# Kernel tuning notes

Hardware: AMD Instinct MI355X
Metric: run time of the kernel (lower is better)

The kernel has to match this reference:

```python
import jax, jax.numpy as jnp
import numpy as np

K = 512        # num_embeddings
D = 64         # embedding_dim
BETA = 0.25
B, S = 64, 4096


def setup_inputs() -> dict:
    key = jax.random.key(0)
    k1, k2 = jax.random.split(key)
    latents = jax.random.normal(k1, (B, S, D), dtype=jnp.float32)
    # torch init: uniform_(-1/K, 1/K)
    embedding = jax.random.uniform(k2, (K, D), dtype=jnp.float32,
                                   minval=-1.0 / K, maxval=1.0 / K)
    return {"latents": latents, "embedding": embedding}


def reference(latents, embedding):
    d = embedding.shape[1]
    flat = latents.reshape(-1, d)                       # [N, D]
    # squared-euclidean distances via norm expansion: [N, K]
    dist = (jnp.sum(flat * flat, axis=1, keepdims=True)
            + jnp.sum(embedding * embedding, axis=1)
            - 2.0 * flat @ embedding.T)
    inds = jnp.argmin(dist, axis=1)                     # [N] (channel = identity)
    # one-hot @ codebook == gather; same math, no [N,K] one-hot materialized
    quantized = embedding[inds].reshape(latents.shape)  # [B, S, D]
    commitment_loss = jnp.mean((jax.lax.stop_gradient(quantized) - latents) ** 2)
    embedding_loss = jnp.mean((quantized - jax.lax.stop_gradient(latents)) ** 2)
    vq_loss = commitment_loss * BETA + embedding_loss
    # straight-through estimator
    quantized_st = latents + jax.lax.stop_gradient(quantized - latents)
    return quantized_st, vq_loss
```

## Files before the change

kernel.cpp:

```cpp
#include <hip/hip_runtime.h>
#include <math.h>
#include <stdint.h>

#define KCODES 512
#define DIM 64
#define NROWS (64 * 4096)
#define BLOCK 512
#define GROUP_ROWS 32
#define ROWS_PER_WAVE 64
#define BM ((BLOCK / 64) * ROWS_PER_WAVE)
#define NBLK (NROWS / BM)

typedef __bf16 bf16x8 __attribute__((ext_vector_type(8)));
typedef float f32x4 __attribute__((ext_vector_type(4)));

typedef __attribute__((address_space(3))) uint32_t* lds_ptr_t;
typedef const __attribute__((address_space(1))) uint32_t* glb_ptr_t;

__global__ void vq_prep_kernel(const float* __restrict__ emb,
                               float* __restrict__ en1,
                               __bf16* __restrict__ ebf) {
    int k = blockIdx.x * blockDim.x + threadIdx.x;
    if (k >= KCODES) return;
    const float4* e4 = reinterpret_cast<const float4*>(emb + k * DIM);
    float s0 = 0.f, s1 = 0.f, s2 = 0.f, s3 = 0.f;
#pragma unroll
    for (int j = 0; j < 8; ++j) {
        float4 v0 = e4[j * 2];
        float4 v1 = e4[j * 2 + 1];
        s0 = fmaf(v0.x, v0.x, s0); s1 = fmaf(v0.y, v0.y, s1);
        s2 = fmaf(v0.z, v0.z, s2); s3 = fmaf(v0.w, v0.w, s3);
        s0 = fmaf(v1.x, v1.x, s0); s1 = fmaf(v1.y, v1.y, s1);
        s2 = fmaf(v1.z, v1.z, s2); s3 = fmaf(v1.w, v1.w, s3);
        bf16x8 p;
        p[0] = (__bf16)(-2.f * v0.x); p[1] = (__bf16)(-2.f * v0.y);
        p[2] = (__bf16)(-2.f * v0.z); p[3] = (__bf16)(-2.f * v0.w);
        p[4] = (__bf16)(-2.f * v1.x); p[5] = (__bf16)(-2.f * v1.y);
        p[6] = (__bf16)(-2.f * v1.z); p[7] = (__bf16)(-2.f * v1.w);
        *reinterpret_cast<bf16x8*>(&ebf[k * DIM + (j ^ (k & 7)) * 8]) = p;
    }
    en1[k] = 1.0f + (s0 + s1) + (s2 + s3);
}

__launch_bounds__(BLOCK, 4)
__global__ void vq_mfma_kernel(const float* __restrict__ lat,
                               const float* __restrict__ emb,
                               const float* __restrict__ en1,
                               const __bf16* __restrict__ ebf,
                               float* __restrict__ outq,
                               float* __restrict__ partials) {
    __shared__ __align__(16) __bf16 e_lds[KCODES * DIM];
    __shared__ float en_lds[KCODES];
    __shared__ float wsum_lds[BLOCK / 64];

    const int t = threadIdx.x;
    const int lane = t & 63, wid = t >> 6;
    const int l15 = lane & 15, lq = lane >> 4;
    const int swz = l15 & 7;
    const uint32_t waverow = (uint32_t)blockIdx.x * BM + (uint32_t)wid * ROWS_PER_WAVE;

#pragma unroll
    for (int i = 0; i < 8; ++i) {
        int c = t + i * BLOCK;
        __builtin_amdgcn_global_load_lds(
            (glb_ptr_t)(const void*)(ebf + c * 8),
            (lds_ptr_t)(void*)(&e_lds[c * 8]), 16, 0, 0);
    }

    float4 araw[2][2][2];
    auto load_a = [&](int g) {
#pragma unroll
        for (int mf = 0; mf < 2; ++mf)
#pragma unroll
            for (int ks = 0; ks < 2; ++ks) {
                const float* xp = lat +
                    (waverow + (uint32_t)g * GROUP_ROWS + mf * 16 + l15) * DIM +
                    ks * 32 + lq * 8;
                araw[mf][ks][0] = reinterpret_cast<const float4*>(xp)[0];
                araw[mf][ks][1] = reinterpret_cast<const float4*>(xp)[1];
            }
    };

    load_a(0);
    en_lds[t] = en1[t];
    __syncthreads();

    float xsq = 0.f, lsum = 0.f;
    bf16x8 afrag[2][2];
    uint32_t best[2][4];

    auto cvt_a = [&]() {
#pragma unroll
        for (int mf = 0; mf < 2; ++mf)
#pragma unroll
            for (int ks = 0; ks < 2; ++ks) {
                float4 v0 = araw[mf][ks][0], v1 = araw[mf][ks][1];
                xsq = fmaf(v0.x, v0.x, xsq); xsq = fmaf(v0.y, v0.y, xsq);
                xsq = fmaf(v0.z, v0.z, xsq); xsq = fmaf(v0.w, v0.w, xsq);
                xsq = fmaf(v1.x, v1.x, xsq); xsq = fmaf(v1.y, v1.y, xsq);
                xsq = fmaf(v1.z, v1.z, xsq); xsq = fmaf(v1.w, v1.w, xsq);
                bf16x8 a;
                a[0] = (__bf16)v0.x; a[1] = (__bf16)v0.y;
                a[2] = (__bf16)v0.z; a[3] = (__bf16)v0.w;
                a[4] = (__bf16)v1.x; a[5] = (__bf16)v1.y;
                a[6] = (__bf16)v1.z; a[7] = (__bf16)v1.w;
                afrag[mf][ks] = a;
            }
    };

    auto score = [&]() {
#pragma unroll
        for (int mf = 0; mf < 2; ++mf)
#pragma unroll
            for (int r = 0; r < 4; ++r) best[mf][r] = 0xFFFFFFFFu;
#pragma unroll 4
        for (int nf = 0; nf < 32; ++nf) {
            const int n = nf * 16 + l15;
            bf16x8 b0 = *reinterpret_cast<const bf16x8*>(
                &e_lds[n * DIM + (lq ^ swz) * 8]);
            bf16x8 b1 = *reinterpret_cast<const bf16x8*>(
                &e_lds[n * DIM + ((lq + 4) ^ swz) * 8]);
            float en = en_lds[n];
            f32x4 acc0 = {en, en, en, en};
            f32x4 acc1 = {en, en, en, en};
            acc0 = __builtin_amdgcn_mfma_f32_16x16x32_bf16(afrag[0][0], b0, acc0, 0, 0, 0);
            acc0 = __builtin_amdgcn_mfma_f32_16x16x32_bf16(afrag[0][1], b1, acc0, 0, 0, 0);
            acc1 = __builtin_amdgcn_mfma_f32_16x16x32_bf16(afrag[1][0], b0, acc1, 0, 0, 0);
            acc1 = __builtin_amdgcn_mfma_f32_16x16x32_bf16(afrag[1][1], b1, acc1, 0, 0, 0);
            const uint32_t nn = (uint32_t)n;
#pragma unroll
            for (int r = 0; r < 4; ++r) {
                uint32_t k0 = (__float_as_uint(acc0[r]) & 0xFFFFFE00u) | nn;
                uint32_t k1 = (__float_as_uint(acc1[r]) & 0xFFFFFE00u) | nn;
                best[0][r] = min(best[0][r], k0);
                best[1][r] = min(best[1][r], k1);
            }
        }
    };

    auto finish = [&](int g) {
#pragma unroll
        for (int off = 1; off < 16; off <<= 1) {
#pragma unroll
            for (int mf = 0; mf < 2; ++mf)
#pragma unroll
                for (int r = 0; r < 4; ++r) {
                    uint32_t o = (uint32_t)__shfl_xor((int)best[mf][r], off, 64);
                    best[mf][r] = min(best[mf][r], o);
                }
        }
        if (l15 == 0) {
#pragma unroll
            for (int mf = 0; mf < 2; ++mf)
#pragma unroll
                for (int r = 0; r < 4; ++r)
                    lsum += __uint_as_float(best[mf][r] & 0xFFFFFE00u) - 1.0f;
        }
        const float4* emb4 = reinterpret_cast<const float4*>(emb);
        float4* out4 = reinterpret_cast<float4*>(outq);
#pragma unroll
        for (int mf = 0; mf < 2; ++mf) {
#pragma unroll
            for (int r = 0; r < 4; ++r) {
                const uint32_t k = best[mf][r] & 511u;
                const uint32_t grow =
                    waverow + (uint32_t)g * GROUP_ROWS + mf * 16 + lq * 4 + r;
                float4 e4 = emb4[k * 16 + l15];
                out4[grow * 16 + l15] = e4;
            }
        }
    };

    cvt_a();
    load_a(1);
    score();
    finish(0);
    cvt_a();
    score();
    finish(1);

    lsum += xsq;

#pragma unroll
    for (int off = 32; off > 0; off >>= 1)
        lsum += __shfl_down(lsum, off, 64);
    if (lane == 0) wsum_lds[wid] = lsum;
    __syncthreads();
    if (t == 0) {
        float s = 0.f;
#pragma unroll
        for (int w = 0; w < BLOCK / 64; ++w) s += wsum_lds[w];
        partials[blockIdx.x] = s;
    }
}

__global__ void vq_loss_kernel(const float* __restrict__ partials,
                               float* __restrict__ loss) {
    float s = 0.f;
    for (int i = threadIdx.x; i < NBLK; i += 256) s += partials[i];
#pragma unroll
    for (int off = 32; off > 0; off >>= 1)
        s += __shfl_down(s, off, 64);
    __shared__ float wsum[4];
    const int lane = threadIdx.x & 63;
    const int wid = threadIdx.x >> 6;
    if (lane == 0) wsum[wid] = s;
    __syncthreads();
    if (threadIdx.x == 0) {
        float tsum = 0.f;
#pragma unroll
        for (int w = 0; w < 4; ++w) tsum += wsum[w];
        loss[0] = 1.25f * (tsum / (float)((size_t)NROWS * DIM));
    }
}

extern "C" void kernel_launch(void* const* d_in, const int* in_sizes, int n_in,
                              void* d_out, int out_size, void* d_ws, size_t ws_size,
                              hipStream_t stream) {
    const float* lat = (const float*)d_in[0];
    const float* emb = (const float*)d_in[1];
    float* outq = (float*)d_out;
    float* loss = (float*)d_out + (size_t)NROWS * DIM;

    float* en1 = (float*)d_ws;
    __bf16* ebf = (__bf16*)((char*)d_ws + 2048);
    float* partials = (float*)((char*)d_ws + 67584);

    vq_prep_kernel<<<2, 256, 0, stream>>>(emb, en1, ebf);
    vq_mfma_kernel<<<NBLK, BLOCK, 0, stream>>>(lat, emb, en1, ebf, outq, partials);
    vq_loss_kernel<<<1, 256, 0, stream>>>(partials, loss);
}
```

Before: 40.90 us.

## Split codebook gather into separate kernel via stored best-code indices

The score kernel no longer writes quantized rows. It stores a 16-bit best-code index per row in workspace, and a new grid-stride gather kernel reads those indices and writes the embedding rows with coalesced float4 stores. The aim is to take the scattered output writes out of the compute-heavy MFMA kernel so it can overlap better, and to let the gather run at full memory bandwidth. The cost is an extra kernel launch plus a small index round-trip through memory.

```diff
diff --git a/kernel.cpp b/kernel.cpp
--- a/kernel.cpp
+++ b/kernel.cpp
@@ -10,6 +10,10 @@
 #define ROWS_PER_WAVE 64
 #define BM ((BLOCK / 64) * ROWS_PER_WAVE)
 #define NBLK (NROWS / BM)
+
+#define GBLOCK 256
+#define GGRID 2048
+#define GCHUNKS 8
 
 typedef __bf16 bf16x8 __attribute__((ext_vector_type(8)));
 typedef float f32x4 __attribute__((ext_vector_type(4)));
@@ -43,12 +47,11 @@
 }
 
 __launch_bounds__(BLOCK, 4)
-__global__ void vq_mfma_kernel(const float* __restrict__ lat,
-                               const float* __restrict__ emb,
-                               const float* __restrict__ en1,
-                               const __bf16* __restrict__ ebf,
-                               float* __restrict__ outq,
-                               float* __restrict__ partials) {
+__global__ void vq_score_kernel(const float* __restrict__ lat,
+                                const float* __restrict__ en1,
+                                const __bf16* __restrict__ ebf,
+                                ushort* __restrict__ bestk,
+                                float* __restrict__ partials) {
     __shared__ __align__(16) __bf16 e_lds[KCODES * DIM];
     __shared__ float en_lds[KCODES];
     __shared__ float wsum_lds[BLOCK / 64];
@@ -150,23 +153,18 @@
                 }
         }
         if (l15 == 0) {
-#pragma unroll
-            for (int mf = 0; mf < 2; ++mf)
+            const uint32_t rbase = waverow + (uint32_t)g * GROUP_ROWS + lq * 4;
+#pragma unroll
+            for (int mf = 0; mf < 2; ++mf) {
 #pragma unroll
                 for (int r = 0; r < 4; ++r)
                     lsum += __uint_as_float(best[mf][r] & 0xFFFFFE00u) - 1.0f;
-        }
-        const float4* emb4 = reinterpret_cast<const float4*>(emb);
-        float4* out4 = reinterpret_cast<float4*>(outq);
-#pragma unroll
-        for (int mf = 0; mf < 2; ++mf) {
-#pragma unroll
-            for (int r = 0; r < 4; ++r) {
-                const uint32_t k = best[mf][r] & 511u;
-                const uint32_t grow =
-                    waverow + (uint32_t)g * GROUP_ROWS + mf * 16 + lq * 4 + r;
-                float4 e4 = emb4[k * 16 + l15];
-                out4[grow * 16 + l15] = e4;
+                ushort4 s;
+                s.x = (ushort)(best[mf][0] & 511u);
+                s.y = (ushort)(best[mf][1] & 511u);
+                s.z = (ushort)(best[mf][2] & 511u);
+                s.w = (ushort)(best[mf][3] & 511u);
+                *reinterpret_cast<ushort4*>(&bestk[rbase + mf * 16]) = s;
             }
         }
     };
@@ -191,6 +189,34 @@
 #pragma unroll
         for (int w = 0; w < BLOCK / 64; ++w) s += wsum_lds[w];
         partials[blockIdx.x] = s;
+    }
+}
+
+__launch_bounds__(GBLOCK, 8)
+__global__ void vq_gather_kernel(const ushort* __restrict__ bestk,
+                                 const float* __restrict__ emb,
+                                 float* __restrict__ outq) {
+    const uint32_t tid = blockIdx.x * GBLOCK + threadIdx.x;
+    const uint32_t stride = GGRID * GBLOCK;
+    const float4* emb4 = reinterpret_cast<const float4*>(emb);
+    float4* out4 = reinterpret_cast<float4*>(outq);
+
+    uint32_t kk[GCHUNKS];
+#pragma unroll
+    for (int i = 0; i < GCHUNKS; ++i) {
+        uint32_t c = tid + i * stride;
+        kk[i] = bestk[c >> 4];
+    }
+    float4 v[GCHUNKS];
+#pragma unroll
+    for (int i = 0; i < GCHUNKS; ++i) {
+        uint32_t c = tid + i * stride;
+        v[i] = emb4[kk[i] * 16u + (c & 15u)];
+    }
+#pragma unroll
+    for (int i = 0; i < GCHUNKS; ++i) {
+        uint32_t c = tid + i * stride;
+        out4[c] = v[i];
     }
 }
 
@@ -225,8 +251,10 @@
     float* en1 = (float*)d_ws;
     __bf16* ebf = (__bf16*)((char*)d_ws + 2048);
     float* partials = (float*)((char*)d_ws + 67584);
+    ushort* bestk = (ushort*)((char*)d_ws + 69632);
 
     vq_prep_kernel<<<2, 256, 0, stream>>>(emb, en1, ebf);
-    vq_mfma_kernel<<<NBLK, BLOCK, 0, stream>>>(lat, emb, en1, ebf, outq, partials);
+    vq_score_kernel<<<NBLK, BLOCK, 0, stream>>>(lat, en1, ebf, bestk, partials);
+    vq_gather_kernel<<<GGRID, GBLOCK, 0, stream>>>(bestk, emb, outq);
     vq_loss_kernel<<<1, 256, 0, stream>>>(partials, loss);
 }
```

Measured after the change: 49.54 us. 21.1% more time.

## Score 64 rows per wave in one pass with 256-thread blocks and block remap

Applied to the files above, without the earlier changes.

Each wave now loads all 64 rows up front and scores them against the codebook in a single pass with four M-fragments, so each LDS B-fragment read feeds twice as many MFMAs. The block shrinks to 256 threads (so the codebook LDS fill loop doubles per thread), occupancy bounds drop to 2, and block IDs are permuted in an interleaved pattern. This removes the two-group software pipeline and doubles per-block codebook LDS loads relative to rows, at the cost of more registers and less latency hiding of the latent loads.

```diff
diff --git a/kernel.cpp b/kernel.cpp
--- a/kernel.cpp
+++ b/kernel.cpp
@@ -5,8 +5,7 @@
 #define KCODES 512
 #define DIM 64
 #define NROWS (64 * 4096)
-#define BLOCK 512
-#define GROUP_ROWS 32
+#define BLOCK 256
 #define ROWS_PER_WAVE 64
 #define BM ((BLOCK / 64) * ROWS_PER_WAVE)
 #define NBLK (NROWS / BM)
@@ -42,7 +41,7 @@
     en1[k] = 1.0f + (s0 + s1) + (s2 + s3);
 }
 
-__launch_bounds__(BLOCK, 4)
+__launch_bounds__(BLOCK, 2)
 __global__ void vq_mfma_kernel(const float* __restrict__ lat,
                                const float* __restrict__ emb,
                                const float* __restrict__ en1,
@@ -57,127 +56,112 @@
     const int lane = t & 63, wid = t >> 6;
     const int l15 = lane & 15, lq = lane >> 4;
     const int swz = l15 & 7;
-    const uint32_t waverow = (uint32_t)blockIdx.x * BM + (uint32_t)wid * ROWS_PER_WAVE;
-
-#pragma unroll
-    for (int i = 0; i < 8; ++i) {
+
+    const uint32_t bid = (blockIdx.x & 7) * (NBLK / 8) + (blockIdx.x >> 3);
+    const uint32_t waverow = bid * BM + (uint32_t)wid * ROWS_PER_WAVE;
+
+#pragma unroll
+    for (int i = 0; i < 16; ++i) {
         int c = t + i * BLOCK;
         __builtin_amdgcn_global_load_lds(
             (glb_ptr_t)(const void*)(ebf + c * 8),
             (lds_ptr_t)(void*)(&e_lds[c * 8]), 16, 0, 0);
     }
 
-    float4 araw[2][2][2];
-    auto load_a = [&](int g) {
-#pragma unroll
-        for (int mf = 0; mf < 2; ++mf)
-#pragma unroll
-            for (int ks = 0; ks < 2; ++ks) {
-                const float* xp = lat +
-                    (waverow + (uint32_t)g * GROUP_ROWS + mf * 16 + l15) * DIM +
-                    ks * 32 + lq * 8;
-                araw[mf][ks][0] = reinterpret_cast<const float4*>(xp)[0];
-                araw[mf][ks][1] = reinterpret_cast<const float4*>(xp)[1];
+    float4 araw[4][2][2];
+#pragma unroll
+    for (int mf = 0; mf < 4; ++mf) {
+#pragma unroll
+        for (int ks = 0; ks < 2; ++ks) {
+            const float* xp = lat +
+                (waverow + mf * 16 + l15) * DIM + ks * 32 + lq * 8;
+            araw[mf][ks][0] = reinterpret_cast<const float4*>(xp)[0];
+            araw[mf][ks][1] = reinterpret_cast<const float4*>(xp)[1];
+        }
+    }
+    en_lds[t] = en1[t];
+    en_lds[t + BLOCK] = en1[t + BLOCK];
+    __syncthreads();
+
+    float xsq = 0.f, lsum = 0.f;
+    bf16x8 afrag[4][2];
+#pragma unroll
+    for (int mf = 0; mf < 4; ++mf) {
+#pragma unroll
+        for (int ks = 0; ks < 2; ++ks) {
+            float4 v0 = araw[mf][ks][0], v1 = araw[mf][ks][1];
+            xsq = fmaf(v0.x, v0.x, xsq); xsq = fmaf(v0.y, v0.y, xsq);
+            xsq = fmaf(v0.z, v0.z, xsq); xsq = fmaf(v0.w, v0.w, xsq);
+            xsq = fmaf(v1.x, v1.x, xsq); xsq = fmaf(v1.y, v1.y, xsq);
+            xsq = fmaf(v1.z, v1.z, xsq); xsq = fmaf(v1.w, v1.w, xsq);
+            bf16x8 a;
+            a[0] = (__bf16)v0.x; a[1] = (__bf16)v0.y;
+            a[2] = (__bf16)v0.z; a[3] = (__bf16)v0.w;
+            a[4] = (__bf16)v1.x; a[5] = (__bf16)v1.y;
+            a[6] = (__bf16)v1.z; a[7] = (__bf16)v1.w;
+            afrag[mf][ks] = a;
+        }
+    }
+
+    uint32_t best[4][4];
+#pragma unroll
+    for (int mf = 0; mf < 4; ++mf)
+#pragma unroll
+        for (int r = 0; r < 4; ++r) best[mf][r] = 0xFFFFFFFFu;
+
+#pragma unroll 4
+    for (int nf = 0; nf < 32; ++nf) {
+        const int n = nf * 16 + l15;
+        bf16x8 b0 = *reinterpret_cast<const bf16x8*>(
+            &e_lds[n * DIM + (lq ^ swz) * 8]);
+        bf16x8 b1 = *reinterpret_cast<const bf16x8*>(
+            &e_lds[n * DIM + ((lq + 4) ^ swz) * 8]);
+        float en = en_lds[n];
+        const uint32_t nn = (uint32_t)n;
+#pragma unroll
+        for (int mf = 0; mf < 4; ++mf) {
+            f32x4 acc = {en, en, en, en};
+            acc = __builtin_amdgcn_mfma_f32_16x16x32_bf16(afrag[mf][0], b0, acc, 0, 0, 0);
+            acc = __builtin_amdgcn_mfma_f32_16x16x32_bf16(afrag[mf][1], b1, acc, 0, 0, 0);
+#pragma unroll
+            for (int r = 0; r < 4; ++r) {
+                uint32_t k = (__float_as_uint(acc[r]) & 0xFFFFFE00u) | nn;
+                best[mf][r] = min(best[mf][r], k);
             }
-    };
-
-    load_a(0);
-    en_lds[t] = en1[t];
-    __syncthreads();
-
-    float xsq = 0.f, lsum = 0.f;
-    bf16x8 afrag[2][2];
-    uint32_t best[2][4];
-
-    auto cvt_a = [&]() {
-#pragma unroll
-        for (int mf = 0; mf < 2; ++mf)
-#pragma unroll
-            for (int ks = 0; ks < 2; ++ks) {
-                float4 v0 = araw[mf][ks][0], v1 = araw[mf][ks][1];
-                xsq = fmaf(v0.x, v0.x, xsq); xsq = fmaf(v0.y, v0.y, xsq);
-                xsq = fmaf(v0.z, v0.z, xsq); xsq = fmaf(v0.w, v0.w, xsq);
-                xsq = fmaf(v1.x, v1.x, xsq); xsq = fmaf(v1.y, v1.y, xsq);
-                xsq = fmaf(v1.z, v1.z, xsq); xsq = fmaf(v1.w, v1.w, xsq);
-                bf16x8 a;
-                a[0] = (__bf16)v0.x; a[1] = (__bf16)v0.y;
-                a[2] = (__bf16)v0.z; a[3] = (__bf16)v0.w;
-                a[4] = (__bf16)v1.x; a[5] = (__bf16)v1.y;
-                a[6] = (__bf16)v1.z; a[7] = (__bf16)v1.w;
-                afrag[mf][ks] = a;
+        }
+    }
+
+#pragma unroll
+    for (int off = 1; off < 16; off <<= 1) {
+#pragma unroll
+        for (int mf = 0; mf < 4; ++mf)
+#pragma unroll
+            for (int r = 0; r < 4; ++r) {
+                uint32_t o = (uint32_t)__shfl_xor((int)best[mf][r], off, 64);
+                best[mf][r] = min(best[mf][r], o);
             }
-    };
-
-    auto score = [&]() {
-#pragma unroll
-        for (int mf = 0; mf < 2; ++mf)
-#pragma unroll
-            for (int r = 0; r < 4; ++r) best[mf][r] = 0xFFFFFFFFu;
-#pragma unroll 4
-        for (int nf = 0; nf < 32; ++nf) {
-            const int n = nf * 16 + l15;
-            bf16x8 b0 = *reinterpret_cast<const bf16x8*>(
-                &e_lds[n * DIM + (lq ^ swz) * 8]);
-            bf16x8 b1 = *reinterpret_cast<const bf16x8*>(
-                &e_lds[n * DIM + ((lq + 4) ^ swz) * 8]);
-            float en = en_lds[n];
-            f32x4 acc0 = {en, en, en, en};
-            f32x4 acc1 = {en, en, en, en};
-            acc0 = __builtin_amdgcn_mfma_f32_16x16x32_bf16(afrag[0][0], b0, acc0, 0, 0, 0);
-            acc0 = __builtin_amdgcn_mfma_f32_16x16x32_bf16(afrag[0][1], b1, acc0, 0, 0, 0);
-            acc1 = __builtin_amdgcn_mfma_f32_16x16x32_bf16(afrag[1][0], b0, acc1, 0, 0, 0);
-            acc1 = __builtin_amdgcn_mfma_f32_16x16x32_bf16(afrag[1][1], b1, acc1, 0, 0, 0);
-            const uint32_t nn = (uint32_t)n;
-#pragma unroll
-            for (int r = 0; r < 4; ++r) {
-                uint32_t k0 = (__float_as_uint(acc0[r]) & 0xFFFFFE00u) | nn;
-                uint32_t k1 = (__float_as_uint(acc1[r]) & 0xFFFFFE00u) | nn;
-                best[0][r] = min(best[0][r], k0);
-                best[1][r] = min(best[1][r], k1);
-            }
-        }
-    };
-
-    auto finish = [&](int g) {
-#pragma unroll
-        for (int off = 1; off < 16; off <<= 1) {
-#pragma unroll
-            for (int mf = 0; mf < 2; ++mf)
-#pragma unroll
-                for (int r = 0; r < 4; ++r) {
-                    uint32_t o = (uint32_t)__shfl_xor((int)best[mf][r], off, 64);
-                    best[mf][r] = min(best[mf][r], o);
-                }
-        }
-        if (l15 == 0) {
-#pragma unroll
-            for (int mf = 0; mf < 2; ++mf)
-#pragma unroll
-                for (int r = 0; r < 4; ++r)
-                    lsum += __uint_as_float(best[mf][r] & 0xFFFFFE00u) - 1.0f;
-        }
-        const float4* emb4 = reinterpret_cast<const float4*>(emb);
-        float4* out4 = reinterpret_cast<float4*>(outq);
-#pragma unroll
-        for (int mf = 0; mf < 2; ++mf) {
-#pragma unroll
-            for (int r = 0; r < 4; ++r) {
-                const uint32_t k = best[mf][r] & 511u;
-                const uint32_t grow =
-                    waverow + (uint32_t)g * GROUP_ROWS + mf * 16 + lq * 4 + r;
-                float4 e4 = emb4[k * 16 + l15];
-                out4[grow * 16 + l15] = e4;
-            }
-        }
-    };
-
-    cvt_a();
-    load_a(1);
-    score();
-    finish(0);
-    cvt_a();
-    score();
-    finish(1);
+    }
+
+    if (l15 == 0) {
+#pragma unroll
+        for (int mf = 0; mf < 4; ++mf)
+#pragma unroll
+            for (int r = 0; r < 4; ++r)
+                lsum += __uint_as_float(best[mf][r] & 0xFFFFFE00u) - 1.0f;
+    }
+
+    const float4* emb4 = reinterpret_cast<const float4*>(emb);
+    float4* out4 = reinterpret_cast<float4*>(outq);
+#pragma unroll
+    for (int mf = 0; mf < 4; ++mf) {
+#pragma unroll
+        for (int r = 0; r < 4; ++r) {
+            const uint32_t k = best[mf][r] & 511u;
+            const uint32_t grow = waverow + mf * 16 + lq * 4 + r;
+            float4 e4 = emb4[k * 16 + l15];
+            out4[grow * 16 + l15] = e4;
+        }
+    }
 
     lsum += xsq;
 
```

New measurement: 47.42 us. 1.16x slower.
